# Kernel optimization log

Hardware: AMD Instinct MI355X
Metric: run time of the kernel (lower is better)

Reference implementation:

```python
import jax, jax.numpy as jnp
import numpy as np

B, S, D, H = 2, 2048, 1024, 16
DK = D // H  # 64


def setup_inputs() -> dict:
    key = jax.random.key(0)
    ks = jax.random.split(key, 9)
    s = 0.02
    return {
        "embeddings": jax.random.normal(ks[0], (B, S, D), jnp.float32),
        "Wq": jax.random.normal(ks[1], (H, D, DK), jnp.float32) * s,
        "bq": jax.random.normal(ks[2], (H, DK), jnp.float32) * s,
        "Wk": jax.random.normal(ks[3], (H, D, DK), jnp.float32) * s,
        "bk": jax.random.normal(ks[4], (H, DK), jnp.float32) * s,
        "Wv": jax.random.normal(ks[5], (H, D, DK), jnp.float32) * s,
        "bv": jax.random.normal(ks[6], (H, DK), jnp.float32) * s,
        "Wo": jax.random.normal(ks[7], (D, D), jnp.float32) * s,
        "bo": jax.random.normal(ks[8], (D,), jnp.float32) * s,
    }


def reference(embeddings, Wq, bq, Wk, bk, Wv, bv, Wo, bo):
    b, s, d = embeddings.shape
    dk = Wq.shape[-1]
    # batched per-head projections: [b,s,d] x [h,d,k] -> [b,h,s,k]
    q = jnp.einsum('bsd,hdk->bhsk', embeddings, Wq) + bq[None, :, None, :]
    k = jnp.einsum('bsd,hdk->bhsk', embeddings, Wk) + bk[None, :, None, :]
    v = jnp.einsum('bsd,hdk->bhsk', embeddings, Wv) + bv[None, :, None, :]
    scores = jnp.einsum('bhqk,bhsk->bhqs', q, k) / jnp.sqrt(jnp.float32(dk))
    causal_mask = jnp.triu(jnp.ones((s, s), dtype=bool), k=1)  # True above diagonal
    scores = jnp.where(causal_mask, jnp.float32(-1e9), scores)
    weights = jax.nn.softmax(scores, axis=-1)
    ctx = jnp.einsum('bhqs,bhsk->bhqk', weights, v)
    concat = ctx.transpose(0, 2, 1, 3).reshape(b, s, d)  # head-major concat, matches torch.cat
    return concat @ Wo + bo
```

## Files before the change

kernel.cpp:

```cpp
#include <hip/hip_runtime.h>
#include <hip/hip_bf16.h>

typedef unsigned short u16;
typedef unsigned int u32;
typedef __bf16 bf16x8 __attribute__((ext_vector_type(8)));
typedef float f32x4 __attribute__((ext_vector_type(4)));
typedef float f32x16 __attribute__((ext_vector_type(16)));

#define AS1 __attribute__((address_space(1)))
#define AS3 __attribute__((address_space(3)))

#define NB 2
#define NS 2048
#define ND 1024
#define NH 16
#define NK 64

__device__ __forceinline__ u16 f2bf(float f) {
  u32 u = __builtin_bit_cast(u32, f);
  return (u16)((u + 0x7FFFu + ((u >> 16) & 1u)) >> 16);
}

__device__ __forceinline__ u32 cvt_pk_bf16(float lo, float hi) {
  u32 u;
  asm("v_cvt_pk_bf16_f32 %0, %1, %2" : "=v"(u) : "v"(lo), "v"(hi));
  return u;
}

__device__ __forceinline__ void stage_tile(u16* lds, const u16* __restrict__ src, int rs,
                                           int wid, int lane) {
#pragma unroll
  for (int i = 0; i < 2; ++i) {
    int c = wid * 128 + i * 64 + lane;
    int row = c >> 3;
    int kc = (c & 7) ^ (row & 7);
    __builtin_amdgcn_global_load_lds((const AS1 u32*)(src + (size_t)row * rs + kc * 8),
                                     (AS3 u32*)(lds + (wid * 128 + i * 64) * 8), 16, 0, 0);
  }
}

__device__ __forceinline__ void stage_warp(u16* lds, const u16* __restrict__ src, int rs,
                                           int lane) {
#pragma unroll
  for (int i = 0; i < 8; ++i) {
    int c = i * 64 + lane;
    int row = c >> 3;
    int kc = (c & 7) ^ (row & 7);
    __builtin_amdgcn_global_load_lds((const AS1 u32*)(src + (size_t)row * rs + kc * 8),
                                     (AS3 u32*)(lds + i * 512), 16, 0, 0);
  }
}

__device__ __forceinline__ bf16x8 read_slot(const u16* lds, int row, int slot) {
  return *(const bf16x8*)(lds + row * 64 + (slot ^ (row & 7)) * 8);
}

__device__ __forceinline__ bf16x8 read_frag(const u16* lds, int row, int ks, int lane) {
  int slot = ((lane >> 4) + ks * 4) ^ (row & 7);
  return *(const bf16x8*)(lds + row * 64 + slot * 8);
}

__global__ __launch_bounds__(256) void convert_kernel(const float* __restrict__ src,
                                                      u16* __restrict__ dst, int n) {
  int i = (blockIdx.x * 256 + threadIdx.x) * 4;
  if (i >= n) return;
  float4 v = *(const float4*)(src + i);
  u32 w0 = cvt_pk_bf16(v.x, v.y);
  u32 w1 = cvt_pk_bf16(v.z, v.w);
  uint2 w; w.x = w0; w.y = w1;
  *(uint2*)(dst + i) = w;
}

__global__ __launch_bounds__(256) void transpose_conv(const float* __restrict__ src,
                                                      u16* __restrict__ dst, int R, int C) {
  __shared__ float tile[32][33];
  size_t base = (size_t)blockIdx.z * R * C;
  src += base;
  dst += base;
  int c0 = blockIdx.x * 32, r0 = blockIdx.y * 32;
  int tx = threadIdx.x, ty = threadIdx.y;
#pragma unroll
  for (int i = 0; i < 4; ++i)
    tile[ty + 8 * i][tx] = src[(size_t)(r0 + ty + 8 * i) * C + c0 + tx];
  __syncthreads();
#pragma unroll
  for (int i = 0; i < 4; ++i)
    dst[(size_t)(c0 + ty + 8 * i) * R + r0 + tx] = f2bf(tile[tx][ty + 8 * i]);
}

template <int MODE>
__global__ __launch_bounds__(256) void gemm128(const u16* __restrict__ A,
                                               const u16* __restrict__ Bt,
                                               const float* __restrict__ b0,
                                               const float* __restrict__ b1,
                                               const float* __restrict__ b2,
                                               u16* __restrict__ Qo, u16* __restrict__ Ko,
                                               u16* __restrict__ Vo,
                                               float* __restrict__ out) {
  __shared__ alignas(16) u16 lds_a[128 * 64];
  __shared__ alignas(16) u16 lds_b[128 * 64];
  int tid = threadIdx.x, lane = tid & 63, wid = tid >> 6;
  int wm = wid >> 1, wn = wid & 1;
  int m0 = blockIdx.x * 128, n0 = blockIdx.y * 128;
  int col = lane & 15;
  f32x4 zero4 = {0.f, 0.f, 0.f, 0.f};
  f32x4 acc[4][4];
#pragma unroll
  for (int i = 0; i < 4; ++i)
#pragma unroll
    for (int j = 0; j < 4; ++j) acc[i][j] = zero4;
  for (int k0 = 0; k0 < ND; k0 += 64) {
    stage_tile(lds_a, A + (size_t)m0 * ND + k0, ND, wid, lane);
    stage_tile(lds_a + 4096, A + (size_t)(m0 + 64) * ND + k0, ND, wid, lane);
    stage_tile(lds_b, Bt + (size_t)n0 * ND + k0, ND, wid, lane);
    stage_tile(lds_b + 4096, Bt + (size_t)(n0 + 64) * ND + k0, ND, wid, lane);
    __syncthreads();
#pragma unroll
    for (int ks = 0; ks < 2; ++ks) {
      bf16x8 af[4], bf[4];
#pragma unroll
      for (int i = 0; i < 4; ++i) af[i] = read_frag(lds_a, wm * 64 + i * 16 + col, ks, lane);
#pragma unroll
      for (int j = 0; j < 4; ++j) bf[j] = read_frag(lds_b, wn * 64 + j * 16 + col, ks, lane);
#pragma unroll
      for (int i = 0; i < 4; ++i)
#pragma unroll
        for (int j = 0; j < 4; ++j)
          acc[i][j] = __builtin_amdgcn_mfma_f32_16x16x32_bf16(af[i], bf[j], acc[i][j], 0, 0, 0);
    }
    __syncthreads();
  }
  int rbase = m0 + wm * 64 + (lane >> 4) * 4;
#pragma unroll
  for (int j = 0; j < 4; ++j) {
    int n = n0 + wn * 64 + j * 16 + col;
    if constexpr (MODE == 0) {
      int which = n >> 10, hh = (n >> 6) & 15, dk = n & 63;
      const float* bp = which == 0 ? b0 : which == 1 ? b1 : b2;
      float bn = bp[hh * 64 + dk];
      if (which == 0) {
#pragma unroll
        for (int i = 0; i < 4; ++i)
#pragma unroll
          for (int r = 0; r < 4; ++r) {
            int m = rbase + i * 16 + r;
            int bb = m >> 11, s = m & (NS - 1);
            Qo[((size_t)(bb * NH + hh) * NS + s) * NK + dk] =
                f2bf((acc[i][j][r] + bn) * 0.18033688f);
          }
      } else if (which == 1) {
#pragma unroll
        for (int i = 0; i < 4; ++i)
#pragma unroll
          for (int r = 0; r < 4; ++r) {
            int m = rbase + i * 16 + r;
            int bb = m >> 11, s = m & (NS - 1);
            Ko[((size_t)(bb * NH + hh) * NS + s) * NK + dk] = f2bf(acc[i][j][r] + bn);
          }
      } else {
#pragma unroll
        for (int i = 0; i < 4; ++i)
#pragma unroll
          for (int r = 0; r < 4; ++r) {
            int m = rbase + i * 16 + r;
            int bb = m >> 11, s = m & (NS - 1);
            int ss = (s & ~12) | ((s & 4) << 1) | ((s & 8) >> 1);
            Vo[((size_t)(bb * NH + hh) * NK + dk) * NS + ss] = f2bf(acc[i][j][r] + bn);
          }
      }
    } else {
      float bn = b0[n];
#pragma unroll
      for (int i = 0; i < 4; ++i)
#pragma unroll
        for (int r = 0; r < 4; ++r)
          out[(size_t)(rbase + i * 16 + r) * ND + n] = acc[i][j][r] + bn;
    }
  }
}

__global__ __launch_bounds__(128, 2) void attn_kernel(const u16* __restrict__ Q,
                                                      const u16* __restrict__ K,
                                                      const u16* __restrict__ Vt,
                                                      u16* __restrict__ ctx) {
  __shared__ alignas(16) u16 ldsK[2][2][4096];
  __shared__ float slab[2][32];
  int tid = threadIdx.x, lane = tid & 63, w = tid >> 6;
  int hi = lane >> 5, ln = lane & 31;
  int bh = blockIdx.x;
  int qt = blockIdx.y;
  const u16* Qb = Q + bh * (NS * NK);
  const u16* Kb = K + bh * (NS * NK);
  const u16* Vb = Vt + bh * (NK * NS);
  int b = bh >> 4, h = bh & 15;
  u16* myK0 = &ldsK[w][0][0];
  u16* myK1 = &ldsK[w][1][0];

  int q0w = qt * 64 + w * 32;
  int qg = q0w + ln;
  bf16x8 qf[4];
#pragma unroll
  for (int ks = 0; ks < 4; ++ks)
    qf[ks] = *(const bf16x8*)(Qb + qg * NK + ks * 16 + hi * 8);

  f32x16 acc0, acc1;
#pragma unroll
  for (int r = 0; r < 16; ++r) { acc0[r] = 0.f; acc1[r] = 0.f; }
  float lp = 0.f;
  int nt = qt + 1;

  stage_warp(myK0, Kb, NK, lane);
  if (nt > 1) stage_warp(myK1, Kb + 64 * NK, NK, lane);

#pragma unroll 1
  for (int t = 0; t < nt; ++t) {
    const u16* lk = (t & 1) ? myK1 : myK0;
    if (t + 1 < nt) {
      asm volatile("s_waitcnt vmcnt(8)" ::: "memory");
    } else {
      asm volatile("s_waitcnt vmcnt(0)" ::: "memory");
    }
    __builtin_amdgcn_sched_barrier(0);
    const u16* Vtb_ = Vb + t * 64;
    bf16x8 vf0[4], vf1[4];
#pragma unroll
    for (int ks = 0; ks < 4; ++ks) {
      vf0[ks] = *(const bf16x8*)(Vtb_ + (size_t)ln * NS + (2 * ks + hi) * 8);
      vf1[ks] = *(const bf16x8*)(Vtb_ + (size_t)(32 + ln) * NS + (2 * ks + hi) * 8);
    }
    f32x16 sc0, sc1;
#pragma unroll
    for (int r = 0; r < 16; ++r) { sc0[r] = 0.f; sc1[r] = 0.f; }
    __builtin_amdgcn_s_setprio(1);
#pragma unroll
    for (int ks = 0; ks < 4; ++ks) {
      bf16x8 kf0 = read_slot(lk, ln, 2 * ks + hi);
      sc0 = __builtin_amdgcn_mfma_f32_32x32x16_bf16(kf0, qf[ks], sc0, 0, 0, 0);
      bf16x8 kf1 = read_slot(lk, 32 + ln, 2 * ks + hi);
      sc1 = __builtin_amdgcn_mfma_f32_32x32x16_bf16(kf1, qf[ks], sc1, 0, 0, 0);
    }
    __builtin_amdgcn_s_setprio(0);
    if (t == qt) {
#pragma unroll
      for (int r = 0; r < 16; ++r) {
        int kl = t * 64 + (r & 3) + 8 * (r >> 2) + 4 * hi;
        if (kl > qg) sc0[r] = -1e30f;
        if (kl + 32 > qg) sc1[r] = -1e30f;
      }
    }
    float ps[4] = {0.f, 0.f, 0.f, 0.f};
#pragma unroll
    for (int r = 0; r < 16; ++r) {
      float p = exp2f(sc0[r]);
      sc0[r] = p;
      ps[r & 3] += p;
    }
#pragma unroll
    for (int r = 0; r < 16; ++r) {
      float p = exp2f(sc1[r]);
      sc1[r] = p;
      ps[r & 3] += p;
    }
    lp += (ps[0] + ps[1]) + (ps[2] + ps[3]);
    u32 wd[8];
    bf16x8 pa[4];
#pragma unroll
    for (int i = 0; i < 8; ++i) wd[i] = cvt_pk_bf16(sc0[2 * i], sc0[2 * i + 1]);
    { uint4 q4; q4.x = wd[0]; q4.y = wd[1]; q4.z = wd[2]; q4.w = wd[3];
      pa[0] = __builtin_bit_cast(bf16x8, q4);
      q4.x = wd[4]; q4.y = wd[5]; q4.z = wd[6]; q4.w = wd[7];
      pa[1] = __builtin_bit_cast(bf16x8, q4); }
#pragma unroll
    for (int i = 0; i < 8; ++i) wd[i] = cvt_pk_bf16(sc1[2 * i], sc1[2 * i + 1]);
    { uint4 q4; q4.x = wd[0]; q4.y = wd[1]; q4.z = wd[2]; q4.w = wd[3];
      pa[2] = __builtin_bit_cast(bf16x8, q4);
      q4.x = wd[4]; q4.y = wd[5]; q4.z = wd[6]; q4.w = wd[7];
      pa[3] = __builtin_bit_cast(bf16x8, q4); }
    __builtin_amdgcn_s_setprio(1);
#pragma unroll
    for (int ks = 0; ks < 4; ++ks) {
      acc0 = __builtin_amdgcn_mfma_f32_32x32x16_bf16(pa[ks], vf0[ks], acc0, 0, 0, 0);
      acc1 = __builtin_amdgcn_mfma_f32_32x32x16_bf16(pa[ks], vf1[ks], acc1, 0, 0, 0);
    }
    __builtin_amdgcn_s_setprio(0);
    if (t + 2 < nt) {
      asm volatile("s_waitcnt lgkmcnt(0)" ::: "memory");
      __builtin_amdgcn_sched_barrier(0);
      stage_warp((t & 1) ? myK1 : myK0, Kb + (t + 2) * 64 * NK, NK, lane);
    }
  }
  lp += __shfl_xor(lp, 32);
  if (!hi) slab[w][ln] = 1.0f / lp;
  float iv[16];
#pragma unroll
  for (int r = 0; r < 16; ++r) iv[r] = slab[w][(r & 3) + 8 * (r >> 2) + 4 * hi];
#pragma unroll
  for (int r = 0; r < 16; ++r) {
    int qq = q0w + (r & 3) + 8 * (r >> 2) + 4 * hi;
    size_t base = (size_t)(b * NS + qq) * ND + h * NK + ln;
    ctx[base] = f2bf(acc0[r] * iv[r]);
    ctx[base + 32] = f2bf(acc1[r] * iv[r]);
  }
}

extern "C" void kernel_launch(void* const* d_in, const int* in_sizes, int n_in,
                              void* d_out, int out_size, void* d_ws, size_t ws_size,
                              hipStream_t stream) {
  (void)in_sizes; (void)n_in; (void)out_size;
  const float* emb = (const float*)d_in[0];
  const float* Wq = (const float*)d_in[1];
  const float* bq = (const float*)d_in[2];
  const float* Wk = (const float*)d_in[3];
  const float* bk = (const float*)d_in[4];
  const float* Wv = (const float*)d_in[5];
  const float* bv = (const float*)d_in[6];
  const float* Wo = (const float*)d_in[7];
  const float* bo = (const float*)d_in[8];
  float* out = (float*)d_out;

  const size_t EMB_N = (size_t)NB * NS * ND;
  const size_t W_N = (size_t)NH * ND * NK;
  const size_t QKV_N = (size_t)NB * NH * NS * NK;
  if (ws_size < (EMB_N + 4 * W_N + 3 * QKV_N) * sizeof(u16)) return;
  u16* ws = (u16*)d_ws;
  u16* emb_bf = ws;
  u16* Wqt = emb_bf + EMB_N;
  u16* Wkt = Wqt + W_N;
  u16* Wvt = Wkt + W_N;
  u16* Wot = Wvt + W_N;
  u16* Qb = Wot + W_N;
  u16* Kb = Qb + QKV_N;
  u16* Vtb = Kb + QKV_N;
  u16* ctxb = emb_bf;

  convert_kernel<<<dim3((int)(EMB_N / 4 / 256)), dim3(256), 0, stream>>>(emb, emb_bf,
                                                                         (int)EMB_N);
  dim3 tb(32, 8);
  transpose_conv<<<dim3(2, 32, 16), tb, 0, stream>>>(Wq, Wqt, ND, NK);
  transpose_conv<<<dim3(2, 32, 16), tb, 0, stream>>>(Wk, Wkt, ND, NK);
  transpose_conv<<<dim3(2, 32, 16), tb, 0, stream>>>(Wv, Wvt, ND, NK);
  transpose_conv<<<dim3(32, 32, 1), tb, 0, stream>>>(Wo, Wot, ND, ND);
  gemm128<0><<<dim3(32, 24), dim3(256), 0, stream>>>(emb_bf, Wqt, bq, bk, bv, Qb, Kb, Vtb,
                                                     nullptr);
  attn_kernel<<<dim3(32, 32), dim3(128), 0, stream>>>(Qb, Kb, Vtb, ctxb);
  gemm128<1><<<dim3(32, 8), dim3(256), 0, stream>>>(ctxb, Wot, bo, nullptr, nullptr,
                                                    nullptr, nullptr, nullptr, out);
}
```

Measured before the change: 148.2 us.

## Split attention into single-wave blocks with reversed query-tile order

The attention kernel now runs one 64-lane wave per block covering 32 query rows, instead of two waves covering 64 rows. The grid doubles and is walked from the longest causal tiles down to the shortest to balance the triangular work. The per-row inverse normaliser now moves through a lane shuffle instead of LDS. The risk is that each wave now stages its own K tiles, so the two waves that used to share a 64-row query tile both load the same K data.

```diff
diff --git a/kernel.cpp b/kernel.cpp
--- a/kernel.cpp
+++ b/kernel.cpp
@@ -179,24 +179,23 @@
   }
 }
 
-__global__ __launch_bounds__(128, 2) void attn_kernel(const u16* __restrict__ Q,
-                                                      const u16* __restrict__ K,
-                                                      const u16* __restrict__ Vt,
-                                                      u16* __restrict__ ctx) {
-  __shared__ alignas(16) u16 ldsK[2][2][4096];
-  __shared__ float slab[2][32];
-  int tid = threadIdx.x, lane = tid & 63, w = tid >> 6;
+__global__ __launch_bounds__(64, 4) void attn_kernel(const u16* __restrict__ Q,
+                                                     const u16* __restrict__ K,
+                                                     const u16* __restrict__ Vt,
+                                                     u16* __restrict__ ctx) {
+  __shared__ alignas(16) u16 ldsK[2][4096];
+  int lane = threadIdx.x & 63;
   int hi = lane >> 5, ln = lane & 31;
   int bh = blockIdx.x;
-  int qt = blockIdx.y;
+  int qt2 = 63 - (int)blockIdx.y;
   const u16* Qb = Q + bh * (NS * NK);
   const u16* Kb = K + bh * (NS * NK);
   const u16* Vb = Vt + bh * (NK * NS);
   int b = bh >> 4, h = bh & 15;
-  u16* myK0 = &ldsK[w][0][0];
-  u16* myK1 = &ldsK[w][1][0];
-
-  int q0w = qt * 64 + w * 32;
+  u16* myK0 = &ldsK[0][0];
+  u16* myK1 = &ldsK[1][0];
+
+  int q0w = qt2 * 32;
   int qg = q0w + ln;
   bf16x8 qf[4];
 #pragma unroll
@@ -207,7 +206,8 @@
 #pragma unroll
   for (int r = 0; r < 16; ++r) { acc0[r] = 0.f; acc1[r] = 0.f; }
   float lp = 0.f;
-  int nt = qt + 1;
+  int tmask = qt2 >> 1;
+  int nt = tmask + 1;
 
   stage_warp(myK0, Kb, NK, lane);
   if (nt > 1) stage_warp(myK1, Kb + 64 * NK, NK, lane);
@@ -240,7 +240,7 @@
       sc1 = __builtin_amdgcn_mfma_f32_32x32x16_bf16(kf1, qf[ks], sc1, 0, 0, 0);
     }
     __builtin_amdgcn_s_setprio(0);
-    if (t == qt) {
+    if (t == tmask) {
 #pragma unroll
       for (int r = 0; r < 16; ++r) {
         int kl = t * 64 + (r & 3) + 8 * (r >> 2) + 4 * hi;
@@ -290,16 +290,15 @@
     }
   }
   lp += __shfl_xor(lp, 32);
-  if (!hi) slab[w][ln] = 1.0f / lp;
-  float iv[16];
-#pragma unroll
-  for (int r = 0; r < 16; ++r) iv[r] = slab[w][(r & 3) + 8 * (r >> 2) + 4 * hi];
+  float inv = 1.0f / lp;
 #pragma unroll
   for (int r = 0; r < 16; ++r) {
-    int qq = q0w + (r & 3) + 8 * (r >> 2) + 4 * hi;
+    int crow = (r & 3) + 8 * (r >> 2) + 4 * hi;
+    float iv = __shfl(inv, crow);
+    int qq = q0w + crow;
     size_t base = (size_t)(b * NS + qq) * ND + h * NK + ln;
-    ctx[base] = f2bf(acc0[r] * iv[r]);
-    ctx[base + 32] = f2bf(acc1[r] * iv[r]);
+    ctx[base] = f2bf(acc0[r] * iv);
+    ctx[base + 32] = f2bf(acc1[r] * iv);
   }
 }
 
@@ -342,7 +341,7 @@
   transpose_conv<<<dim3(32, 32, 1), tb, 0, stream>>>(Wo, Wot, ND, ND);
   gemm128<0><<<dim3(32, 24), dim3(256), 0, stream>>>(emb_bf, Wqt, bq, bk, bv, Qb, Kb, Vtb,
                                                      nullptr);
-  attn_kernel<<<dim3(32, 32), dim3(128), 0, stream>>>(Qb, Kb, Vtb, ctxb);
+  attn_kernel<<<dim3(32, 64), dim3(64), 0, stream>>>(Qb, Kb, Vtb, ctxb);
   gemm128<1><<<dim3(32, 8), dim3(256), 0, stream>>>(ctxb, Wot, bo, nullptr, nullptr,
                                                     nullptr, nullptr, nullptr, out);
 }
```

Measured after the change: 144.1 us. 1.03x faster.
